# Kernel optimization log

Hardware: AMD Instinct MI355X
Metric: run time of the kernel (lower is better)

The kernel has to match this reference:

```python
import jax, jax.numpy as jnp
import numpy as np

D_MODEL, H, D_K = 768, 12, 64
B, S = 2, 2048
NEG = -1.0e9


def setup_inputs() -> dict:
    key = jax.random.key(0)
    ks = jax.random.split(key, 7)
    q = jax.random.normal(ks[0], (B, S, D_MODEL), dtype=jnp.float32)
    k = jax.random.normal(ks[1], (B, S, D_MODEL), dtype=jnp.float32)
    v = jax.random.normal(ks[2], (B, S, D_MODEL), dtype=jnp.float32)
    mask = jnp.tril(jnp.ones((S, S), dtype=jnp.int32))[None, None]  # [1,1,S,S] causal
    sc = 1.0 / np.sqrt(D_MODEL)
    w_q = jax.random.normal(ks[3], (D_MODEL, D_MODEL), dtype=jnp.float32) * sc
    w_k = jax.random.normal(ks[4], (D_MODEL, D_MODEL), dtype=jnp.float32) * sc
    w_v = jax.random.normal(ks[5], (D_MODEL, D_MODEL), dtype=jnp.float32) * sc
    w_o = jax.random.normal(ks[6], (D_MODEL, D_MODEL), dtype=jnp.float32) * sc
    return {"q": q, "k": k, "v": v, "mask": mask,
            "w_q": w_q, "w_k": w_k, "w_v": w_v, "w_o": w_o}


def reference(q, k, v, mask, w_q, w_k, w_v, w_o):
    # nn.Linear(x) = x @ W.T ; split heads: [B,S,D] -> [B,H,S,Dk]
    def split_heads(x, w):
        y = jnp.einsum('bsd,ed->bse', x, w)
        return y.reshape(x.shape[0], x.shape[1], H, D_K).transpose(0, 2, 1, 3)

    qh = split_heads(q, w_q)
    kh = split_heads(k, w_k)
    vh = split_heads(v, w_v)
    scores = jnp.einsum('bhqd,bhkd->bhqk', qh, kh) / jnp.sqrt(jnp.float32(D_K))
    scores = jnp.where(mask == 0, jnp.float32(NEG), scores)
    attn = jax.nn.softmax(scores, axis=-1)  # dropout p=0 -> identity
    ctx = jnp.einsum('bhqk,bhkd->bhqd', attn, vh)
    ctx = ctx.transpose(0, 2, 1, 3).reshape(q.shape[0], q.shape[1], D_MODEL)
    return jnp.einsum('bsd,ed->bse', ctx, w_o)
```

## Files before the change

kernel.cpp:

```cpp
#include <hip/hip_runtime.h>

#define DM   768
#define HN   12
#define DKH  64
#define BSZ  2
#define SEQ  2048
#define MROWS (BSZ*SEQ)
#define NEGBIG -1.0e9f

typedef __bf16 bf16;
typedef __bf16 bf16x8 __attribute__((ext_vector_type(8)));
typedef __bf16 bf16x4 __attribute__((ext_vector_type(4)));
typedef float  f32x4  __attribute__((ext_vector_type(4)));
typedef unsigned int uint32;

__device__ __forceinline__ void gload_lds16(const void* g, void* l) {
    __builtin_amdgcn_global_load_lds(
        (const __attribute__((address_space(1))) char*)g,
        (__attribute__((address_space(3))) char*)l, 16, 0, 0);
}

__global__ __launch_bounds__(256) void cvt3(const float* __restrict__ a, const float* __restrict__ b,
                                            const float* __restrict__ c,
                                            bf16* __restrict__ x, bf16* __restrict__ y,
                                            bf16* __restrict__ z, int n) {
    const float* s; bf16* d;
    if      (blockIdx.y == 0) { s = a; d = x; }
    else if (blockIdx.y == 1) { s = b; d = y; }
    else                      { s = c; d = z; }
    int i = (blockIdx.x * 256 + threadIdx.x) * 4;
    if (i + 3 < n) {
        float4 v = *(const float4*)(s + i);
        bf16x4 o; o[0] = (bf16)v.x; o[1] = (bf16)v.y; o[2] = (bf16)v.z; o[3] = (bf16)v.w;
        *(bf16x4*)(d + i) = o;
    }
}
__global__ __launch_bounds__(256) void cvt4(const float* __restrict__ a, const float* __restrict__ b,
                                            const float* __restrict__ c, const float* __restrict__ e,
                                            bf16* __restrict__ x, bf16* __restrict__ y,
                                            bf16* __restrict__ z, bf16* __restrict__ u, int n) {
    const float* s; bf16* d;
    if      (blockIdx.y == 0) { s = a; d = x; }
    else if (blockIdx.y == 1) { s = b; d = y; }
    else if (blockIdx.y == 2) { s = c; d = z; }
    else                      { s = e; d = u; }
    int i = (blockIdx.x * 256 + threadIdx.x) * 4;
    if (i + 3 < n) {
        float4 v = *(const float4*)(s + i);
        bf16x4 o; o[0] = (bf16)v.x; o[1] = (bf16)v.y; o[2] = (bf16)v.z; o[3] = (bf16)v.w;
        *(bf16x4*)(d + i) = o;
    }
}

__global__ __launch_bounds__(256) void gemm_qkv(
    const bf16* __restrict__ xq, const bf16* __restrict__ xk, const bf16* __restrict__ xv,
    const bf16* __restrict__ wq, const bf16* __restrict__ wk, const bf16* __restrict__ wv,
    bf16* __restrict__ qh, bf16* __restrict__ kh, bf16* __restrict__ vt)
{
    __shared__ bf16 As[128 * 32];
    __shared__ bf16 Bs[128 * 32];

    const bf16* A; const bf16* Bw; bf16* Out;
    if      (blockIdx.z == 0) { A = xq; Bw = wq; Out = qh; }
    else if (blockIdx.z == 1) { A = xk; Bw = wk; Out = kh; }
    else                      { A = xv; Bw = wv; Out = vt; }
    const bool vout = (blockIdx.z == 2);

    const int t = threadIdx.x, w = t >> 6, lane = t & 63;
    const int mt = blockIdx.x * 128, nt = blockIdx.y * 128;
    const int wr = (w >> 1) * 64, wc = (w & 1) * 64;

    f32x4 acc[4][4] = {};

    for (int k0 = 0; k0 < DM; k0 += 32) {
        #pragma unroll
        for (int i = 0; i < 2; i++) {
            int c = i * 256 + t;
            int row = c >> 2, col = (c & 3) * 8;
            gload_lds16(A  + (size_t)(mt + row) * DM + k0 + col, (char*)As + c * 16);
            gload_lds16(Bw + (size_t)(nt + row) * DM + k0 + col, (char*)Bs + c * 16);
        }
        asm volatile("s_waitcnt vmcnt(0)" ::: "memory");
        __syncthreads();

        bf16x8 af[4], bfr[4];
        #pragma unroll
        for (int m = 0; m < 4; m++)
            af[m] = *(const bf16x8*)&As[(wr + m * 16 + (lane & 15)) * 32 + (lane >> 4) * 8];
        #pragma unroll
        for (int n = 0; n < 4; n++)
            bfr[n] = *(const bf16x8*)&Bs[(wc + n * 16 + (lane & 15)) * 32 + (lane >> 4) * 8];
        #pragma unroll
        for (int m = 0; m < 4; m++)
            #pragma unroll
            for (int n = 0; n < 4; n++)
                acc[m][n] = __builtin_amdgcn_mfma_f32_16x16x32_bf16(af[m], bfr[n], acc[m][n], 0, 0, 0);
        __syncthreads();
    }

    if (!vout) {
        #pragma unroll
        for (int m = 0; m < 4; m++) {
            #pragma unroll
            for (int n = 0; n < 4; n++) {
                #pragma unroll
                for (int r = 0; r < 4; r++) {
                    int gm = mt + wr + m * 16 + (lane >> 4) * 4 + r;
                    int gn = nt + wc + n * 16 + (lane & 15);
                    int b = gm >> 11, s = gm & 2047, h = gn >> 6, d = gn & 63;
                    Out[(((size_t)b * HN + h) * SEQ + s) * DKH + d] = (bf16)acc[m][n][r];
                }
            }
        }
    } else {
        #pragma unroll
        for (int m = 0; m < 4; m++) {
            #pragma unroll
            for (int n = 0; n < 4; n++) {
                int gm = mt + wr + m * 16 + (lane >> 4) * 4;
                int gn = nt + wc + n * 16 + (lane & 15);
                int b = gm >> 11, s0 = gm & 2047, h = gn >> 6, d = gn & 63;
                bf16x4 pk;
                #pragma unroll
                for (int r = 0; r < 4; r++) pk[r] = (bf16)acc[m][n][r];
                *(bf16x4*)&Out[(((size_t)b * HN + h) * DKH + d) * SEQ + s0] = pk;
            }
        }
    }
}

__global__ __launch_bounds__(256) void gemm_out(
    const bf16* __restrict__ Actx, const bf16* __restrict__ Bw, float* __restrict__ Out)
{
    __shared__ bf16 As[128 * 32];
    __shared__ bf16 Bs[128 * 32];

    const int t = threadIdx.x, w = t >> 6, lane = t & 63;
    const int mt = blockIdx.x * 128, nt = blockIdx.y * 128;
    const int wr = (w >> 1) * 64, wc = (w & 1) * 64;

    f32x4 acc[4][4] = {};

    for (int k0 = 0; k0 < DM; k0 += 32) {
        #pragma unroll
        for (int i = 0; i < 2; i++) {
            int c = i * 256 + t;
            int row = c >> 2, col = (c & 3) * 8;
            gload_lds16(Actx + (size_t)(mt + row) * DM + k0 + col, (char*)As + c * 16);
            gload_lds16(Bw   + (size_t)(nt + row) * DM + k0 + col, (char*)Bs + c * 16);
        }
        asm volatile("s_waitcnt vmcnt(0)" ::: "memory");
        __syncthreads();

        bf16x8 af[4], bfr[4];
        #pragma unroll
        for (int m = 0; m < 4; m++)
            af[m] = *(const bf16x8*)&As[(wr + m * 16 + (lane & 15)) * 32 + (lane >> 4) * 8];
        #pragma unroll
        for (int n = 0; n < 4; n++)
            bfr[n] = *(const bf16x8*)&Bs[(wc + n * 16 + (lane & 15)) * 32 + (lane >> 4) * 8];
        #pragma unroll
        for (int m = 0; m < 4; m++)
            #pragma unroll
            for (int n = 0; n < 4; n++)
                acc[m][n] = __builtin_amdgcn_mfma_f32_16x16x32_bf16(af[m], bfr[n], acc[m][n], 0, 0, 0);
        __syncthreads();
    }

    #pragma unroll
    for (int m = 0; m < 4; m++) {
        #pragma unroll
        for (int n = 0; n < 4; n++) {
            #pragma unroll
            for (int r = 0; r < 4; r++) {
                int gm = mt + wr + m * 16 + (lane >> 4) * 4 + r;
                int gn = nt + wc + n * 16 + (lane & 15);
                Out[(size_t)gm * DM + gn] = acc[m][n][r];
            }
        }
    }
}

__global__ __launch_bounds__(256, 3) void flash_attn(
    const bf16* __restrict__ qh, const bf16* __restrict__ kh,
    const bf16* __restrict__ vt, bf16* __restrict__ ctx)
{
    __shared__ bf16 Ks[2][4096];
    __shared__ bf16 Vs[2][4096];
    __shared__ bf16 pl[4][32 * 72];

    const int bid = blockIdx.x;
    const int qt = 15 - bid / 24;
    const int bh = bid % 24;
    const int qb = qt * 128;
    const int t = threadIdx.x, w = t >> 6, lane = t & 63;
    const int g = lane >> 4, lo = lane & 15;
    const size_t base = (size_t)bh * SEQ * DKH;
    const char* khead = (const char*)(kh + base);
    const char* vhead = (const char*)(vt + base);

    uint32 koff[2], voff[2];
    #pragma unroll
    for (int i = 0; i < 2; i++) {
        int c = w * 128 + i * 64 + lane;
        int r = c >> 3, s = c & 7;
        int sw = s ^ (r & 7);
        koff[i] = (uint32)(r * 128  + 16 * sw);
        voff[i] = (uint32)(r * 4096 + 16 * sw);
    }
    const uint32 kr0 = (uint32)(128 * lo + 16 * (g ^ (lo & 7)));
    const uint32 kr1 = kr0 ^ 64;

    const int qrow0 = qb + 16 * w + lo;
    const int qrow1 = qb + 64 + 16 * w + lo;
    const bf16* qp0 = qh + base + (size_t)qrow0 * DKH + g * 8;
    const bf16* qp1 = qh + base + (size_t)qrow1 * DKH + g * 8;
    bf16x8 qa0 = *(const bf16x8*)qp0;
    bf16x8 qa1 = *(const bf16x8*)(qp0 + 32);
    bf16x8 qb0 = *(const bf16x8*)qp1;
    bf16x8 qb1 = *(const bf16x8*)(qp1 + 32);

    f32x4 O0[4] = {}, O1[4] = {};
    float m0 = -1e30f, l0 = 0.0f, m1 = -1e30f, l1 = 0.0f;
    bf16* plw = &pl[w][0];

    const int T = 2 * qt + 2;

    #pragma unroll
    for (int i = 0; i < 2; i++) {
        int c16 = (w * 128 + i * 64 + lane) * 16;
        gload_lds16(khead + koff[i], (char*)&Ks[0][0] + c16);
        gload_lds16(vhead + voff[i], (char*)&Vs[0][0] + c16);
    }
    asm volatile("s_waitcnt vmcnt(0)" ::: "memory");
    __syncthreads();

    for (int it = 0; it < T; ++it) {
        const int par = it & 1, nxt = par ^ 1;
        if (it + 1 < T) {
            const char* ks = khead + (size_t)(it + 1) * 8192;
            const char* vs = vhead + (size_t)(it + 1) * 128;
            #pragma unroll
            for (int i = 0; i < 2; i++) {
                int c16 = (w * 128 + i * 64 + lane) * 16;
                gload_lds16(ks + koff[i], (char*)&Ks[nxt][0] + c16);
                gload_lds16(vs + voff[i], (char*)&Vs[nxt][0] + c16);
            }
        }

        const bool act0  = (it != T - 1);
        const bool diag0 = (it == T - 2);
        const bool diag1 = (it == T - 1);

        const char* Kp = (const char*)&Ks[par][0];
        f32x4 s0[4], s1[4];
        {
            bf16x8 kf0[4], kf1[4];
            #pragma unroll
            for (int cg = 0; cg < 4; cg++) {
                kf0[cg] = *(const bf16x8*)(Kp + cg * 2048 + kr0);
                kf1[cg] = *(const bf16x8*)(Kp + cg * 2048 + kr1);
            }
            __builtin_amdgcn_s_setprio(1);
            if (act0) {
                #pragma unroll
                for (int cg = 0; cg < 4; cg++) {
                    f32x4 z = {0.0f, 0.0f, 0.0f, 0.0f};
                    z = __builtin_amdgcn_mfma_f32_16x16x32_bf16(kf0[cg], qa0, z, 0, 0, 0);
                    z = __builtin_amdgcn_mfma_f32_16x16x32_bf16(kf1[cg], qa1, z, 0, 0, 0);
                    s0[cg] = z;
                }
            }
            #pragma unroll
            for (int cg = 0; cg < 4; cg++) {
                f32x4 z = {0.0f, 0.0f, 0.0f, 0.0f};
                z = __builtin_amdgcn_mfma_f32_16x16x32_bf16(kf0[cg], qb0, z, 0, 0, 0);
                z = __builtin_amdgcn_mfma_f32_16x16x32_bf16(kf1[cg], qb1, z, 0, 0, 0);
                s1[cg] = z;
            }
            __builtin_amdgcn_s_setprio(0);
        }

        if (act0) {
            if (diag0) {
                #pragma unroll
                for (int cg = 0; cg < 4; cg++)
                    #pragma unroll
                    for (int r = 0; r < 4; r++) {
                        int ki = it * 64 + cg * 16 + 4 * g + r;
                        float v = s0[cg][r] * 0.125f;
                        s0[cg][r] = (ki > qrow0) ? NEGBIG : v;
                    }
            } else {
                #pragma unroll
                for (int cg = 0; cg < 4; cg++)
                    #pragma unroll
                    for (int r = 0; r < 4; r++) s0[cg][r] *= 0.125f;
            }
        }
        if (diag1) {
            #pragma unroll
            for (int cg = 0; cg < 4; cg++)
                #pragma unroll
                for (int r = 0; r < 4; r++) {
                    int ki = it * 64 + cg * 16 + 4 * g + r;
                    float v = s1[cg][r] * 0.125f;
                    s1[cg][r] = (ki > qrow1) ? NEGBIG : v;
                }
        } else {
            #pragma unroll
            for (int cg = 0; cg < 4; cg++)
                #pragma unroll
                for (int r = 0; r < 4; r++) s1[cg][r] *= 0.125f;
        }

        if (act0) {
            float mx = fmaxf(fmaxf(fmaxf(s0[0][0], s0[0][1]), fmaxf(s0[0][2], s0[0][3])),
                             fmaxf(fmaxf(s0[1][0], s0[1][1]), fmaxf(s0[1][2], s0[1][3])));
            mx = fmaxf(mx, fmaxf(fmaxf(fmaxf(s0[2][0], s0[2][1]), fmaxf(s0[2][2], s0[2][3])),
                                 fmaxf(fmaxf(s0[3][0], s0[3][1]), fmaxf(s0[3][2], s0[3][3]))));
            mx = fmaxf(mx, __shfl_xor(mx, 16, 64));
            mx = fmaxf(mx, __shfl_xor(mx, 32, 64));
            if (!__all(mx - m0 <= 8.0f)) {
                float mnew = fmaxf(m0, mx);
                float scl = __expf(m0 - mnew);
                m0 = mnew; l0 *= scl;
                float s4[4];
                #pragma unroll
                for (int r = 0; r < 4; r++) s4[r] = __shfl(scl, 4 * g + r, 64);
                #pragma unroll
                for (int dg = 0; dg < 4; dg++)
                    #pragma unroll
                    for (int r = 0; r < 4; r++) O0[dg][r] *= s4[r];
            }
            float rs = 0.0f;
            #pragma unroll
            for (int cg = 0; cg < 4; cg++)
                #pragma unroll
                for (int r = 0; r < 4; r++) {
                    s0[cg][r] = __expf(s0[cg][r] - m0);
                    rs += s0[cg][r];
                }
            rs += __shfl_xor(rs, 16, 64);
            rs += __shfl_xor(rs, 32, 64);
            l0 += rs;
            #pragma unroll
            for (int cg = 0; cg < 4; cg++) {
                bf16x4 pk;
                #pragma unroll
                for (int r = 0; r < 4; r++) pk[r] = (bf16)s0[cg][r];
                *(bf16x4*)&plw[lo * 72 + cg * 16 + 4 * g] = pk;
            }
        }
        {
            float mx = fmaxf(fmaxf(fmaxf(s1[0][0], s1[0][1]), fmaxf(s1[0][2], s1[0][3])),
                             fmaxf(fmaxf(s1[1][0], s1[1][1]), fmaxf(s1[1][2], s1[1][3])));
            mx = fmaxf(mx, fmaxf(fmaxf(fmaxf(s1[2][0], s1[2][1]), fmaxf(s1[2][2], s1[2][3])),
                                 fmaxf(fmaxf(s1[3][0], s1[3][1]), fmaxf(s1[3][2], s1[3][3]))));
            mx = fmaxf(mx, __shfl_xor(mx, 16, 64));
            mx = fmaxf(mx, __shfl_xor(mx, 32, 64));
            if (!__all(mx - m1 <= 8.0f)) {
                float mnew = fmaxf(m1, mx);
                float scl = __expf(m1 - mnew);
                m1 = mnew; l1 *= scl;
                float s4[4];
                #pragma unroll
                for (int r = 0; r < 4; r++) s4[r] = __shfl(scl, 4 * g + r, 64);
                #pragma unroll
                for (int dg = 0; dg < 4; dg++)
                    #pragma unroll
                    for (int r = 0; r < 4; r++) O1[dg][r] *= s4[r];
            }
            float rs = 0.0f;
            #pragma unroll
            for (int cg = 0; cg < 4; cg++)
                #pragma unroll
                for (int r = 0; r < 4; r++) {
                    s1[cg][r] = __expf(s1[cg][r] - m1);
                    rs += s1[cg][r];
                }
            rs += __shfl_xor(rs, 16, 64);
            rs += __shfl_xor(rs, 32, 64);
            l1 += rs;
            #pragma unroll
            for (int cg = 0; cg < 4; cg++) {
                bf16x4 pk;
                #pragma unroll
                for (int r = 0; r < 4; r++) pk[r] = (bf16)s1[cg][r];
                *(bf16x4*)&plw[(16 + lo) * 72 + cg * 16 + 4 * g] = pk;
            }
        }

        {
            const char* Vp = (const char*)&Vs[par][0];
            bf16x8 vv[8];
            #pragma unroll
            for (int kq = 0; kq < 2; kq++)
                #pragma unroll
                for (int dblk = 0; dblk < 4; dblk++)
                    vv[kq * 4 + dblk] = *(const bf16x8*)
                        (Vp + (dblk * 16 + lo) * 128 + 16 * ((4 * kq + g) ^ (lo & 7)));
            __builtin_amdgcn_s_setprio(1);
            if (act0) {
                #pragma unroll
                for (int kq = 0; kq < 2; kq++) {
                    bf16x8 pa = *(const bf16x8*)&plw[lo * 72 + kq * 32 + 8 * g];
                    #pragma unroll
                    for (int dblk = 0; dblk < 4; dblk++)
                        O0[dblk] = __builtin_amdgcn_mfma_f32_16x16x32_bf16(pa, vv[kq * 4 + dblk], O0[dblk], 0, 0, 0);
                }
            }
            #pragma unroll
            for (int kq = 0; kq < 2; kq++) {
                bf16x8 pa = *(const bf16x8*)&plw[(16 + lo) * 72 + kq * 32 + 8 * g];
                #pragma unroll
                for (int dblk = 0; dblk < 4; dblk++)
                    O1[dblk] = __builtin_amdgcn_mfma_f32_16x16x32_bf16(pa, vv[kq * 4 + dblk], O1[dblk], 0, 0, 0);
            }
            __builtin_amdgcn_s_setprio(0);
        }

        asm volatile("s_waitcnt vmcnt(0)" ::: "memory");
        __syncthreads();
    }

    const int b = bh / HN, h = bh % HN;
    float inv0[4], inv1[4];
    #pragma unroll
    for (int r = 0; r < 4; r++) {
        inv0[r] = 1.0f / __shfl(l0, 4 * g + r, 64);
        inv1[r] = 1.0f / __shfl(l1, 4 * g + r, 64);
    }
    #pragma unroll
    for (int dg = 0; dg < 4; dg++) {
        #pragma unroll
        for (int r = 0; r < 4; r++) {
            int row0 = qb + 16 * w + g * 4 + r;
            int row1 = qb + 64 + 16 * w + g * 4 + r;
            ctx[((size_t)(b * SEQ + row0)) * DM + h * DKH + dg * 16 + lo] =
                (bf16)(O0[dg][r] * inv0[r]);
            ctx[((size_t)(b * SEQ + row1)) * DM + h * DKH + dg * 16 + lo] =
                (bf16)(O1[dg][r] * inv1[r]);
        }
    }
}

extern "C" void kernel_launch(void* const* d_in, const int* in_sizes, int n_in,
                              void* d_out, int out_size, void* d_ws, size_t ws_size,
                              hipStream_t stream) {
    const float* q  = (const float*)d_in[0];
    const float* k  = (const float*)d_in[1];
    const float* v  = (const float*)d_in[2];
    const float* wq = (const float*)d_in[4];
    const float* wk = (const float*)d_in[5];
    const float* wv = (const float*)d_in[6];
    const float* wo = (const float*)d_in[7];
    float* out = (float*)d_out;

    const size_t NX = (size_t)MROWS * DM;
    const size_t NW = (size_t)DM * DM;

    bf16* p = (bf16*)d_ws;
    bf16* xq  = p; p += NX;
    bf16* xk  = p; p += NX;
    bf16* xv  = p; p += NX;
    bf16* wqb = p; p += NW;
    bf16* wkb = p; p += NW;
    bf16* wvb = p; p += NW;
    bf16* wob = p; p += NW;
    bf16* qhp = p; p += NX;
    bf16* khp = p; p += NX;
    bf16* vtp = p; p += NX;
    bf16* ctxp = p; p += NX;

    cvt3<<<dim3(NX / 1024, 3), 256, 0, stream>>>(q, k, v, xq, xk, xv, (int)NX);
    cvt4<<<dim3(NW / 1024, 4), 256, 0, stream>>>(wq, wk, wv, wo, wqb, wkb, wvb, wob, (int)NW);

    gemm_qkv<<<dim3(MROWS / 128, DM / 128, 3), 256, 0, stream>>>(
        xq, xk, xv, wqb, wkb, wvb, qhp, khp, vtp);

    flash_attn<<<(SEQ / 128) * (BSZ * HN), 256, 0, stream>>>(qhp, khp, vtp, ctxp);

    gemm_out<<<dim3(MROWS / 128, DM / 128), 256, 0, stream>>>(ctxp, wob, out);
}
```

Baseline: 121.6 us.

## Split causal attention KV range across blocks and merge partials in a combine kernel

Replaces the single flash attention kernel with a split-KV version. Long causal query tiles are divided into 2 to 4 key ranges so every block runs at most about 8 key tiles instead of up to 32. Partial outputs, row maxes and row sums go to workspace, reusing the already-consumed xq buffer. A new combine kernel merges them with log-sum-exp weighting. This targets the load imbalance of the causal triangle, at the cost of an extra launch, extra global traffic, and partial outputs rounded to bf16.

```diff
diff --git a/kernel.cpp b/kernel.cpp
--- a/kernel.cpp
+++ b/kernel.cpp
@@ -7,6 +7,7 @@
 #define SEQ  2048
 #define MROWS (BSZ*SEQ)
 #define NEGBIG -1.0e9f
+#define NSLOT 40
 
 typedef __bf16 bf16;
 typedef __bf16 bf16x8 __attribute__((ext_vector_type(8)));
@@ -181,17 +182,30 @@
     }
 }
 
-__global__ __launch_bounds__(256, 3) void flash_attn(
+__global__ __launch_bounds__(256, 3) void flash_split(
     const bf16* __restrict__ qh, const bf16* __restrict__ kh,
-    const bf16* __restrict__ vt, bf16* __restrict__ ctx)
+    const bf16* __restrict__ vt, bf16* __restrict__ ctx,
+    bf16* __restrict__ pO, float* __restrict__ pM, float* __restrict__ pL)
 {
     __shared__ bf16 Ks[2][4096];
     __shared__ bf16 Vs[2][4096];
     __shared__ bf16 pl[4][32 * 72];
 
     const int bid = blockIdx.x;
-    const int qt = 15 - bid / 24;
+    const int slot = bid / 24;
     const int bh = bid % 24;
+
+    int qt, p, np;
+    if (slot < 16)      { qt = 15 - (slot >> 2); p = slot & 3;  np = 4; }
+    else if (slot < 28) { int s = slot - 16; qt = 11 - s / 3; p = s % 3; np = 3; }
+    else if (slot < 36) { int s = slot - 28; qt = 7 - (s >> 1); p = s & 1; np = 2; }
+    else                { qt = 39 - slot; p = 0; np = 1; }
+
+    const int T = 2 * qt + 2;
+    const int bse = T / np, rem = T - bse * np;
+    const int cnt   = bse + (p < rem ? 1 : 0);
+    const int start = p * bse + (p < rem ? p : rem);
+
     const int qb = qt * 128;
     const int t = threadIdx.x, w = t >> 6, lane = t & 63;
     const int g = lane >> 4, lo = lane & 15;
@@ -224,22 +238,21 @@
     float m0 = -1e30f, l0 = 0.0f, m1 = -1e30f, l1 = 0.0f;
     bf16* plw = &pl[w][0];
 
-    const int T = 2 * qt + 2;
-
     #pragma unroll
     for (int i = 0; i < 2; i++) {
         int c16 = (w * 128 + i * 64 + lane) * 16;
-        gload_lds16(khead + koff[i], (char*)&Ks[0][0] + c16);
-        gload_lds16(vhead + voff[i], (char*)&Vs[0][0] + c16);
+        gload_lds16(khead + (size_t)start * 8192 + koff[i], (char*)&Ks[0][0] + c16);
+        gload_lds16(vhead + (size_t)start * 128  + voff[i], (char*)&Vs[0][0] + c16);
     }
     asm volatile("s_waitcnt vmcnt(0)" ::: "memory");
     __syncthreads();
 
-    for (int it = 0; it < T; ++it) {
+    for (int it = 0; it < cnt; ++it) {
+        const int kt = start + it;
         const int par = it & 1, nxt = par ^ 1;
-        if (it + 1 < T) {
-            const char* ks = khead + (size_t)(it + 1) * 8192;
-            const char* vs = vhead + (size_t)(it + 1) * 128;
+        if (it + 1 < cnt) {
+            const char* ks = khead + (size_t)(kt + 1) * 8192;
+            const char* vs = vhead + (size_t)(kt + 1) * 128;
             #pragma unroll
             for (int i = 0; i < 2; i++) {
                 int c16 = (w * 128 + i * 64 + lane) * 16;
@@ -248,9 +261,9 @@
             }
         }
 
-        const bool act0  = (it != T - 1);
-        const bool diag0 = (it == T - 2);
-        const bool diag1 = (it == T - 1);
+        const bool act0  = (kt != T - 1);
+        const bool diag0 = (kt == T - 2);
+        const bool diag1 = (kt == T - 1);
 
         const char* Kp = (const char*)&Ks[par][0];
         f32x4 s0[4], s1[4];
@@ -287,7 +300,7 @@
                 for (int cg = 0; cg < 4; cg++)
                     #pragma unroll
                     for (int r = 0; r < 4; r++) {
-                        int ki = it * 64 + cg * 16 + 4 * g + r;
+                        int ki = kt * 64 + cg * 16 + 4 * g + r;
                         float v = s0[cg][r] * 0.125f;
                         s0[cg][r] = (ki > qrow0) ? NEGBIG : v;
                     }
@@ -303,7 +316,7 @@
             for (int cg = 0; cg < 4; cg++)
                 #pragma unroll
                 for (int r = 0; r < 4; r++) {
-                    int ki = it * 64 + cg * 16 + 4 * g + r;
+                    int ki = kt * 64 + cg * 16 + 4 * g + r;
                     float v = s1[cg][r] * 0.125f;
                     s1[cg][r] = (ki > qrow1) ? NEGBIG : v;
                 }
@@ -424,24 +437,91 @@
         __syncthreads();
     }
 
+    if (np == 1) {
+        const int b = bh / HN, h = bh % HN;
+        float inv0[4], inv1[4];
+        #pragma unroll
+        for (int r = 0; r < 4; r++) {
+            inv0[r] = 1.0f / __shfl(l0, 4 * g + r, 64);
+            inv1[r] = 1.0f / __shfl(l1, 4 * g + r, 64);
+        }
+        #pragma unroll
+        for (int dg = 0; dg < 4; dg++) {
+            #pragma unroll
+            for (int r = 0; r < 4; r++) {
+                int row0 = qb + 16 * w + g * 4 + r;
+                int row1 = qb + 64 + 16 * w + g * 4 + r;
+                ctx[((size_t)(b * SEQ + row0)) * DM + h * DKH + dg * 16 + lo] =
+                    (bf16)(O0[dg][r] * inv0[r]);
+                ctx[((size_t)(b * SEQ + row1)) * DM + h * DKH + dg * 16 + lo] =
+                    (bf16)(O1[dg][r] * inv1[r]);
+            }
+        }
+    } else {
+        const int pslot = bh * NSLOT + slot;
+        bf16* po = pO + (size_t)pslot * 128 * 64;
+        #pragma unroll
+        for (int dg = 0; dg < 4; dg++) {
+            #pragma unroll
+            for (int r = 0; r < 4; r++) {
+                int r0 = 16 * w + 4 * g + r;
+                po[r0 * 64 + dg * 16 + lo]        = (bf16)O0[dg][r];
+                po[(64 + r0) * 64 + dg * 16 + lo] = (bf16)O1[dg][r];
+            }
+        }
+        if (g == 0) {
+            pM[pslot * 128 + 16 * w + lo]      = m0;
+            pL[pslot * 128 + 16 * w + lo]      = l0;
+            pM[pslot * 128 + 64 + 16 * w + lo] = m1;
+            pL[pslot * 128 + 64 + 16 * w + lo] = l1;
+        }
+    }
+}
+
+__global__ __launch_bounds__(256) void flash_combine(
+    const bf16* __restrict__ pO, const float* __restrict__ pM,
+    const float* __restrict__ pL, bf16* __restrict__ ctx)
+{
+    const int bh = blockIdx.x;
+    const int qt = 4 + blockIdx.y;
+    int np, s0;
+    if (qt >= 12)     { np = 4; s0 = (15 - qt) * 4; }
+    else if (qt >= 8) { np = 3; s0 = 16 + (11 - qt) * 3; }
+    else              { np = 2; s0 = 28 + (7 - qt) * 2; }
+
+    const int t = threadIdx.x;
+    const int row = t >> 1, dh = (t & 1) * 32;
+    const int pbase = bh * NSLOT + s0;
+
+    float mi[4], wi[4];
+    float mstar = -1e30f;
+    #pragma unroll
+    for (int i = 0; i < 4; i++)
+        if (i < np) { mi[i] = pM[(pbase + i) * 128 + row]; mstar = fmaxf(mstar, mi[i]); }
+    float lsum = 0.0f;
+    #pragma unroll
+    for (int i = 0; i < 4; i++)
+        if (i < np) { wi[i] = __expf(mi[i] - mstar); lsum += wi[i] * pL[(pbase + i) * 128 + row]; }
+    const float linv = 1.0f / lsum;
+
     const int b = bh / HN, h = bh % HN;
-    float inv0[4], inv1[4];
+    bf16* crow = ctx + ((size_t)(b * SEQ + qt * 128 + row)) * DM + h * DKH + dh;
+
     #pragma unroll
-    for (int r = 0; r < 4; r++) {
-        inv0[r] = 1.0f / __shfl(l0, 4 * g + r, 64);
-        inv1[r] = 1.0f / __shfl(l1, 4 * g + r, 64);
-    }
-    #pragma unroll
-    for (int dg = 0; dg < 4; dg++) {
-        #pragma unroll
-        for (int r = 0; r < 4; r++) {
-            int row0 = qb + 16 * w + g * 4 + r;
-            int row1 = qb + 64 + 16 * w + g * 4 + r;
-            ctx[((size_t)(b * SEQ + row0)) * DM + h * DKH + dg * 16 + lo] =
-                (bf16)(O0[dg][r] * inv0[r]);
-            ctx[((size_t)(b * SEQ + row1)) * DM + h * DKH + dg * 16 + lo] =
-                (bf16)(O1[dg][r] * inv1[r]);
-        }
+    for (int d0 = 0; d0 < 32; d0 += 8) {
+        float acc[8] = {};
+        #pragma unroll
+        for (int i = 0; i < 4; i++) {
+            if (i < np) {
+                bf16x8 o = *(const bf16x8*)&pO[((size_t)(pbase + i) * 128 + row) * 64 + dh + d0];
+                #pragma unroll
+                for (int j = 0; j < 8; j++) acc[j] += wi[i] * (float)o[j];
+            }
+        }
+        bf16x8 ov;
+        #pragma unroll
+        for (int j = 0; j < 8; j++) ov[j] = (bf16)(acc[j] * linv);
+        *(bf16x8*)(crow + d0) = ov;
     }
 }
 
@@ -473,13 +553,18 @@
     bf16* vtp = p; p += NX;
     bf16* ctxp = p; p += NX;
 
+    bf16*  pO = xq;
+    float* pM = (float*)(xq + (size_t)24 * NSLOT * 128 * 64);
+    float* pL = pM + 24 * NSLOT * 128;
+
     cvt3<<<dim3(NX / 1024, 3), 256, 0, stream>>>(q, k, v, xq, xk, xv, (int)NX);
     cvt4<<<dim3(NW / 1024, 4), 256, 0, stream>>>(wq, wk, wv, wo, wqb, wkb, wvb, wob, (int)NW);
 
     gemm_qkv<<<dim3(MROWS / 128, DM / 128, 3), 256, 0, stream>>>(
         xq, xk, xv, wqb, wkb, wvb, qhp, khp, vtp);
 
-    flash_attn<<<(SEQ / 128) * (BSZ * HN), 256, 0, stream>>>(qhp, khp, vtp, ctxp);
+    flash_split<<<24 * NSLOT, 256, 0, stream>>>(qhp, khp, vtp, ctxp, pO, pM, pL);
+    flash_combine<<<dim3(24, 12), 256, 0, stream>>>(pO, pM, pL, ctxp);
 
     gemm_out<<<dim3(MROWS / 128, DM / 128), 256, 0, stream>>>(ctxp, wob, out);
 }
```

Result: faster. 105.7 us (-13.1%).
